# Kernel tuning notes

Measured on AMD Instinct MI355X. Metric: run time of the kernel, lower is better.

Reference implementation:

```python
import jax, jax.numpy as jnp
import numpy as np
from jax import lax

HID, FFN, NUM_EXPERTS, TOP_K = 1024, 4096, 16, 4
B, S = 4, 2048


def setup_inputs() -> dict:
    key = jax.random.key(0)
    ks = jax.random.split(key, 7)
    scale = 0.02
    x = jax.random.normal(ks[0], (B, S, HID), dtype=jnp.float32)
    Wg = jax.random.normal(ks[1], (HID, NUM_EXPERTS), dtype=jnp.float32) * scale
    bg = jnp.zeros((NUM_EXPERTS,), dtype=jnp.float32)
    W1 = jax.random.normal(ks[2], (NUM_EXPERTS, HID, FFN), dtype=jnp.float32) * scale
    b1 = jnp.zeros((NUM_EXPERTS, FFN), dtype=jnp.float32)
    W2 = jax.random.normal(ks[3], (NUM_EXPERTS, FFN, HID), dtype=jnp.float32) * scale
    b2 = jnp.zeros((NUM_EXPERTS, HID), dtype=jnp.float32)
    return {"x": x, "Wg": Wg, "bg": bg, "W1": W1, "b1": b1, "W2": W2, "b2": b2}


def reference(x, Wg, bg, W1, b1, W2, b2):
    b, s, h = x.shape
    xf = x.reshape(-1, h)                                  # [T, H]
    T = xf.shape[0]
    logits = xf @ Wg + bg                                  # [T, E]
    top_w, top_idx = lax.top_k(logits, TOP_K)              # [T, K]
    top_w = jax.nn.softmax(top_w, axis=-1)
    # Dense combine weights [T, E]; topk indices are distinct so add == set.
    combine = jnp.zeros((T, NUM_EXPERTS), dtype=xf.dtype)
    combine = combine.at[jnp.arange(T)[:, None], top_idx].add(top_w)

    def body(acc, params):
        W1e, b1e, W2e, b2e, ce = params                    # ce: [T]
        hdn = jax.nn.gelu(xf @ W1e + b1e, approximate=False)  # [T, F]
        ye = hdn @ W2e + b2e                               # [T, H]
        return acc + ce[:, None] * ye, None

    out, _ = lax.scan(body, jnp.zeros_like(xf), (W1, b1, W2, b2, combine.T))
    return out.reshape(b, s, h)
```

## Files before the change

### kernel.cpp

```cpp
#include <hip/hip_runtime.h>
#include <hip/hip_bf16.h>


#define HID 1024
#define FFN 4096
#define NE 16
#define TOPK 4
#define NTOK 8192
#define NPAIR (NTOK*TOPK)

typedef __attribute__((ext_vector_type(4))) float f32x4;
typedef __attribute__((ext_vector_type(8))) short bf16x8;
typedef unsigned short u16;
typedef unsigned int u32;

__device__ __forceinline__ u16 f2bf(float f){
  u32 u = __float_as_uint(f);
  u32 r = (u + 0x7fffu + ((u >> 16) & 1u)) >> 16;
  return (u16)r;
}

__device__ __forceinline__ void gload_lds16(const void* g, void* l){
  __builtin_amdgcn_global_load_lds((const __attribute__((address_space(1))) void*)g,
                                   (__attribute__((address_space(3))) void*)l, 16, 0, 0);
}

__global__ __launch_bounds__(256) void k_gating(const float* __restrict__ x,
    const float* __restrict__ Wg, const float* __restrict__ bg,
    int* __restrict__ counts, int* __restrict__ tke, float* __restrict__ tkw){
  int t    = (blockIdx.x << 2) + (threadIdx.x >> 6);
  int lane = threadIdx.x & 63;
  const float* xr = x + (size_t)t*HID + lane*16;
  float acc[NE];
  #pragma unroll
  for (int e=0;e<NE;e++) acc[e] = 0.f;
  #pragma unroll
  for (int j=0;j<16;j++){
    float xj = xr[j];
    const float* wr = Wg + (size_t)(lane*16 + j)*NE;
    #pragma unroll
    for (int e=0;e<NE;e++) acc[e] += xj * wr[e];
  }
  #pragma unroll
  for (int off=32; off; off>>=1){
    #pragma unroll
    for (int e=0;e<NE;e++) acc[e] += __shfl_xor(acc[e], off);
  }
  if (lane == 0){
    #pragma unroll
    for (int e=0;e<NE;e++) acc[e] += bg[e];
    int te[TOPK]; float tv[TOPK];
    #pragma unroll
    for (int k=0;k<TOPK;k++){
      int bi = 0; float bv = -1e30f;
      #pragma unroll
      for (int e=0;e<NE;e++) if (acc[e] > bv){ bv = acc[e]; bi = e; }
      te[k] = bi; tv[k] = bv; acc[bi] = -1e30f;
    }
    float m = tv[0], s = 0.f, w[TOPK];
    #pragma unroll
    for (int k=0;k<TOPK;k++){ w[k] = expf(tv[k]-m); s += w[k]; }
    float inv = 1.f/s;
    #pragma unroll
    for (int k=0;k<TOPK;k++){
      tke[t*TOPK+k] = te[k];
      tkw[t*TOPK+k] = w[k]*inv;
      atomicAdd(&counts[te[k]], 1);
    }
  }
}

__global__ void k_scan(const int* __restrict__ counts, int* __restrict__ offsets){
  if (threadIdx.x == 0){
    int a = 0;
    for (int e=0;e<NE;e++){ offsets[e] = a; a += counts[e]; }
    offsets[NE] = a;
  }
}

__global__ __launch_bounds__(256) void k_scatter(const int* __restrict__ tke,
    const float* __restrict__ tkw, const int* __restrict__ offsets,
    int* __restrict__ cursors, int* __restrict__ ltok, float* __restrict__ lw){
  int t = blockIdx.x*256 + threadIdx.x;
  #pragma unroll
  for (int k=0;k<TOPK;k++){
    int e = tke[t*TOPK+k];
    int p = atomicAdd(&cursors[e], 1);
    int r = offsets[e] + p;
    ltok[r] = t;
    lw[r]   = tkw[t*TOPK+k];
  }
}

__global__ __launch_bounds__(256) void k_cvt_x(const float* __restrict__ x, u16* __restrict__ xb){
  size_t i = ((size_t)blockIdx.x*256 + threadIdx.x) * 8;
  const float4* p = (const float4*)(x + i);
  float4 a = p[0], b = p[1];
  uint4 o;
  o.x = f2bf(a.x) | ((u32)f2bf(a.y) << 16);
  o.y = f2bf(a.z) | ((u32)f2bf(a.w) << 16);
  o.z = f2bf(b.x) | ((u32)f2bf(b.y) << 16);
  o.w = f2bf(b.z) | ((u32)f2bf(b.w) << 16);
  *(uint4*)(xb + i) = o;
}

__global__ __launch_bounds__(256) void k_wcvt(const float* __restrict__ src,
    u16* __restrict__ dst, int R, int C){
  int e = blockIdx.z;
  src += (size_t)e*R*C;
  dst += (size_t)e*R*C;
  int c0 = blockIdx.x*64, r0 = blockIdx.y*64;
  __shared__ u16 t[64][72];
  int tid = threadIdx.x;
  #pragma unroll
  for (int it=0; it<4; it++){
    int i  = it*256 + tid;
    int rr = i >> 4;
    int c4 = (i & 15) << 2;
    float4 v = *(const float4*)(src + (size_t)(r0+rr)*C + c0 + c4);
    t[rr][c4+0] = f2bf(v.x);
    t[rr][c4+1] = f2bf(v.y);
    t[rr][c4+2] = f2bf(v.z);
    t[rr][c4+3] = f2bf(v.w);
  }
  __syncthreads();
  #pragma unroll
  for (int it=0; it<2; it++){
    int i   = it*256 + tid;
    int cc  = i >> 3;
    int rr0 = (i & 7) << 3;
    uint4 o;
    o.x = (u32)t[rr0+0][cc] | ((u32)t[rr0+1][cc] << 16);
    o.y = (u32)t[rr0+2][cc] | ((u32)t[rr0+3][cc] << 16);
    o.z = (u32)t[rr0+4][cc] | ((u32)t[rr0+5][cc] << 16);
    o.w = (u32)t[rr0+6][cc] | ((u32)t[rr0+7][cc] << 16);
    *(uint4*)(dst + (size_t)(c0+cc)*R + r0 + rr0) = o;
  }
}

__global__ __launch_bounds__(256) void k_ffn1(
    const u16* __restrict__ xb, const u16* __restrict__ w1t,
    const float* __restrict__ b1,
    const int* __restrict__ counts, const int* __restrict__ offsets,
    const int* __restrict__ ltok, u16* __restrict__ hdn){
  int e = blockIdx.z;
  int cnt = counts[e];
  int row0 = blockIdx.y << 7;
  if (row0 >= cnt) return;
  int n0 = blockIdx.x << 7;
  int soff = offsets[e];
  const int* lt = ltok + soff;

  __shared__ u16 lA[128*64];
  __shared__ u16 lB[128*64];

  int tid = threadIdx.x, lane = tid & 63, wv = tid >> 6;
  int wr = (wv >> 1) << 6, wc = (wv & 1) << 6;
  int l15 = lane & 15, lkhi = (lane >> 4) << 3;

  f32x4 acc[4][4];
  #pragma unroll
  for (int m=0;m<4;m++){
    #pragma unroll
    for (int n=0;n<4;n++) acc[m][n] = (f32x4)0.f;
  }
  const u16* wBp = w1t + ((size_t)e*FFN + n0)*HID;

  for (int k0=0; k0<HID; k0+=64){
    __syncthreads();
    #pragma unroll
    for (int it=0; it<4; it++){
      int idx = it*256 + tid;
      int row = idx >> 3;
      int kc  = ((idx & 7) ^ (row & 7)) << 3;
      int rc = row0 + row; if (rc > cnt-1) rc = cnt-1;
      int tok = lt[rc];
      gload_lds16(xb  + (size_t)tok*HID + k0 + kc, &lA[idx<<3]);
      gload_lds16(wBp + (size_t)row*HID + k0 + kc, &lB[idx<<3]);
    }
    __syncthreads();
    #pragma unroll
    for (int kk=0; kk<64; kk+=32){
      bf16x8 af[4], bfv[4];
      #pragma unroll
      for (int m=0;m<4;m++){
        int ra = wr + m*16 + l15;
        af[m]  = *(const bf16x8*)&lA[ra*64 + ((kk + lkhi) ^ ((ra&7)<<3))];
      }
      #pragma unroll
      for (int n=0;n<4;n++){
        int rb = wc + n*16 + l15;
        bfv[n] = *(const bf16x8*)&lB[rb*64 + ((kk + lkhi) ^ ((rb&7)<<3))];
      }
      #pragma unroll
      for (int m=0;m<4;m++){
        #pragma unroll
        for (int n=0;n<4;n++)
          acc[m][n] = __builtin_amdgcn_mfma_f32_16x16x32_bf16(af[m], bfv[n], acc[m][n], 0,0,0);
      }
    }
  }
  int rhi = (lane >> 4) << 2;
  #pragma unroll
  for (int m=0;m<4;m++){
    int rl = wr + m*16 + rhi;
    #pragma unroll
    for (int j=0;j<4;j++){
      int row = row0 + rl + j;
      if (row < cnt){
        size_t base = (size_t)(soff + row)*FFN;
        #pragma unroll
        for (int n=0;n<4;n++){
          int col = n0 + wc + n*16 + l15;
          float z = acc[m][n][j] + b1[(size_t)e*FFN + col];
          float g = 0.5f*z*(1.0f + erff(z*0.70710678118654752f));
          hdn[base + col] = f2bf(g);
        }
      }
    }
  }
}

__global__ __launch_bounds__(256) void k_ffn2(
    const u16* __restrict__ hdn, const u16* __restrict__ w2t,
    const float* __restrict__ b2,
    const int* __restrict__ counts, const int* __restrict__ offsets,
    const int* __restrict__ ltok, const float* __restrict__ lw,
    float* __restrict__ out){
  int e = blockIdx.z;
  int cnt = counts[e];
  int row0 = blockIdx.y << 7;
  if (row0 >= cnt) return;
  int n0 = blockIdx.x << 7;
  int soff = offsets[e];

  __shared__ u16 lA[128*64];
  __shared__ u16 lB[128*64];

  int tid = threadIdx.x, lane = tid & 63, wv = tid >> 6;
  int wr = (wv >> 1) << 6, wc = (wv & 1) << 6;
  int l15 = lane & 15, lkhi = (lane >> 4) << 3;

  f32x4 acc[4][4];
  #pragma unroll
  for (int m=0;m<4;m++){
    #pragma unroll
    for (int n=0;n<4;n++) acc[m][n] = (f32x4)0.f;
  }
  const u16* wBp = w2t + ((size_t)e*HID + n0)*FFN;

  for (int k0=0; k0<FFN; k0+=64){
    __syncthreads();
    #pragma unroll
    for (int it=0; it<4; it++){
      int idx = it*256 + tid;
      int row = idx >> 3;
      int kc  = ((idx & 7) ^ (row & 7)) << 3;
      int rc = row0 + row; if (rc > cnt-1) rc = cnt-1;
      gload_lds16(hdn + (size_t)(soff+rc)*FFN + k0 + kc, &lA[idx<<3]);
      gload_lds16(wBp + (size_t)row*FFN     + k0 + kc, &lB[idx<<3]);
    }
    __syncthreads();
    #pragma unroll
    for (int kk=0; kk<64; kk+=32){
      bf16x8 af[4], bfv[4];
      #pragma unroll
      for (int m=0;m<4;m++){
        int ra = wr + m*16 + l15;
        af[m]  = *(const bf16x8*)&lA[ra*64 + ((kk + lkhi) ^ ((ra&7)<<3))];
      }
      #pragma unroll
      for (int n=0;n<4;n++){
        int rb = wc + n*16 + l15;
        bfv[n] = *(const bf16x8*)&lB[rb*64 + ((kk + lkhi) ^ ((rb&7)<<3))];
      }
      #pragma unroll
      for (int m=0;m<4;m++){
        #pragma unroll
        for (int n=0;n<4;n++)
          acc[m][n] = __builtin_amdgcn_mfma_f32_16x16x32_bf16(af[m], bfv[n], acc[m][n], 0,0,0);
      }
    }
  }
  int rhi = (lane >> 4) << 2;
  #pragma unroll
  for (int m=0;m<4;m++){
    int rl = wr + m*16 + rhi;
    #pragma unroll
    for (int j=0;j<4;j++){
      int row = row0 + rl + j;
      if (row < cnt){
        float sw = lw[soff+row];
        int tok  = ltok[soff+row];
        float* orow = out + (size_t)tok*HID;
        #pragma unroll
        for (int n=0;n<4;n++){
          int col = n0 + wc + n*16 + l15;
          atomicAdd(orow + col, sw*(acc[m][n][j] + b2[(size_t)e*HID + col]));
        }
      }
    }
  }
}

extern "C" void kernel_launch(void* const* d_in, const int* in_sizes, int n_in,
                              void* d_out, int out_size, void* d_ws, size_t ws_size,
                              hipStream_t stream){
  const float* x  = (const float*)d_in[0];
  const float* Wg = (const float*)d_in[1];
  const float* bg = (const float*)d_in[2];
  const float* W1 = (const float*)d_in[3];
  const float* b1 = (const float*)d_in[4];
  const float* W2 = (const float*)d_in[5];
  const float* b2 = (const float*)d_in[6];
  float* out = (float*)d_out;

  char* ws = (char*)d_ws;
  size_t off = 0;
  u16* SLOT_A = (u16*)(ws + off); off += (size_t)NE*FFN*HID*2;
  u16* XB  = (u16*)(ws + off); off += (size_t)NTOK*HID*2;
  u16* HDN = (u16*)(ws + off); off += (size_t)NPAIR*FFN*2;
  int*   LTOK = (int*)(ws + off);   off += (size_t)NPAIR*4;
  float* LW   = (float*)(ws + off); off += (size_t)NPAIR*4;
  int*   TKE  = (int*)(ws + off);   off += (size_t)NPAIR*4;
  float* TKW  = (float*)(ws + off); off += (size_t)NPAIR*4;
  int*   CTRL = (int*)(ws + off);   off += 256;
  int* counts  = CTRL;
  int* offsets = CTRL + 16;
  int* cursors = CTRL + 33;

  (void)hipMemsetAsync(CTRL, 0, 256, stream);
  (void)hipMemsetAsync(out, 0, (size_t)NTOK*HID*sizeof(float), stream);

  k_gating<<<NTOK/4, 256, 0, stream>>>(x, Wg, bg, counts, TKE, TKW);
  k_scan<<<1, 64, 0, stream>>>(counts, offsets);
  k_scatter<<<NTOK/256, 256, 0, stream>>>(TKE, TKW, offsets, cursors, LTOK, LW);
  k_cvt_x<<<(NTOK*HID/8)/256, 256, 0, stream>>>(x, XB);
  k_wcvt<<<dim3(FFN/64, HID/64, NE), 256, 0, stream>>>(W1, SLOT_A, HID, FFN);
  k_ffn1<<<dim3(FFN/128, NTOK/128, NE), 256, 0, stream>>>(XB, SLOT_A, b1, counts, offsets, LTOK, HDN);
  k_wcvt<<<dim3(HID/64, FFN/64, NE), 256, 0, stream>>>(W2, SLOT_A, FFN, HID);
  k_ffn2<<<dim3(HID/128, NTOK/128, NE), 256, 0, stream>>>(HDN, SLOT_A, b2, counts, offsets, LTOK, LW, out);
}
```

Baseline: 2.298 ms.

## Double-buffer LDS tiles in both expert FFN GEMM kernels to overlap loads

Both grouped GEMM kernels now use two LDS buffers per operand. Each iteration issues the global-to-LDS loads for the next K tile before running the MFMAs on the current one, and synchronises once per iteration instead of twice. Per-thread gather offsets, including the token index lookup, are precomputed once outside the K loop. LDS use doubles to 64 KB per block, which may cut the number of resident blocks. Correctness depends on the compiler's waitcnt handling of async LDS loads at the barrier.

Result: no change. 2.323 ms (+1.1%).

```diff
diff --git a/kernel.cpp b/kernel.cpp
--- a/kernel.cpp
+++ b/kernel.cpp
@@ -151,8 +151,8 @@
   int soff = offsets[e];
   const int* lt = ltok + soff;
 
-  __shared__ u16 lA[128*64];
-  __shared__ u16 lB[128*64];
+  __shared__ u16 lA[2][128*64];
+  __shared__ u16 lB[2][128*64];
 
   int tid = threadIdx.x, lane = tid & 63, wv = tid >> 6;
   int wr = (wv >> 1) << 6, wc = (wv & 1) << 6;
@@ -166,31 +166,43 @@
   }
   const u16* wBp = w1t + ((size_t)e*FFN + n0)*HID;
 
-  for (int k0=0; k0<HID; k0+=64){
-    __syncthreads();
+  size_t aoff[4], boff[4];
+  #pragma unroll
+  for (int it=0; it<4; it++){
+    int idx = it*256 + tid;
+    int row = idx >> 3;
+    int kc  = ((idx & 7) ^ (row & 7)) << 3;
+    int rc = row0 + row; if (rc > cnt-1) rc = cnt-1;
+    aoff[it] = (size_t)lt[rc]*HID + kc;
+    boff[it] = (size_t)row*HID + kc;
+  }
+
+  auto stage = [&](int buf, int k0v){
     #pragma unroll
     for (int it=0; it<4; it++){
       int idx = it*256 + tid;
-      int row = idx >> 3;
-      int kc  = ((idx & 7) ^ (row & 7)) << 3;
-      int rc = row0 + row; if (rc > cnt-1) rc = cnt-1;
-      int tok = lt[rc];
-      gload_lds16(xb  + (size_t)tok*HID + k0 + kc, &lA[idx<<3]);
-      gload_lds16(wBp + (size_t)row*HID + k0 + kc, &lB[idx<<3]);
-    }
-    __syncthreads();
+      gload_lds16(xb  + aoff[it] + k0v, &lA[buf][idx<<3]);
+      gload_lds16(wBp + boff[it] + k0v, &lB[buf][idx<<3]);
+    }
+  };
+
+  stage(0, 0);
+  __syncthreads();
+  int cur = 0;
+  for (int t=0; t<HID/64; ++t){
+    if (t+1 < HID/64) stage(cur^1, (t+1)*64);
     #pragma unroll
     for (int kk=0; kk<64; kk+=32){
       bf16x8 af[4], bfv[4];
       #pragma unroll
       for (int m=0;m<4;m++){
         int ra = wr + m*16 + l15;
-        af[m]  = *(const bf16x8*)&lA[ra*64 + ((kk + lkhi) ^ ((ra&7)<<3))];
+        af[m]  = *(const bf16x8*)&lA[cur][ra*64 + ((kk + lkhi) ^ ((ra&7)<<3))];
       }
       #pragma unroll
       for (int n=0;n<4;n++){
         int rb = wc + n*16 + l15;
-        bfv[n] = *(const bf16x8*)&lB[rb*64 + ((kk + lkhi) ^ ((rb&7)<<3))];
+        bfv[n] = *(const bf16x8*)&lB[cur][rb*64 + ((kk + lkhi) ^ ((rb&7)<<3))];
       }
       #pragma unroll
       for (int m=0;m<4;m++){
@@ -199,6 +211,8 @@
           acc[m][n] = __builtin_amdgcn_mfma_f32_16x16x32_bf16(af[m], bfv[n], acc[m][n], 0,0,0);
       }
     }
+    __syncthreads();
+    cur ^= 1;
   }
   int rhi = (lane >> 4) << 2;
   #pragma unroll
@@ -234,8 +248,8 @@
   int n0 = blockIdx.x << 7;
   int soff = offsets[e];
 
-  __shared__ u16 lA[128*64];
-  __shared__ u16 lB[128*64];
+  __shared__ u16 lA[2][128*64];
+  __shared__ u16 lB[2][128*64];
 
   int tid = threadIdx.x, lane = tid & 63, wv = tid >> 6;
   int wr = (wv >> 1) << 6, wc = (wv & 1) << 6;
@@ -249,30 +263,43 @@
   }
   const u16* wBp = w2t + ((size_t)e*HID + n0)*FFN;
 
-  for (int k0=0; k0<FFN; k0+=64){
-    __syncthreads();
+  size_t aoff[4], boff[4];
+  #pragma unroll
+  for (int it=0; it<4; it++){
+    int idx = it*256 + tid;
+    int row = idx >> 3;
+    int kc  = ((idx & 7) ^ (row & 7)) << 3;
+    int rc = row0 + row; if (rc > cnt-1) rc = cnt-1;
+    aoff[it] = (size_t)(soff+rc)*FFN + kc;
+    boff[it] = (size_t)row*FFN + kc;
+  }
+
+  auto stage = [&](int buf, int k0v){
     #pragma unroll
     for (int it=0; it<4; it++){
       int idx = it*256 + tid;
-      int row = idx >> 3;
-      int kc  = ((idx & 7) ^ (row & 7)) << 3;
-      int rc = row0 + row; if (rc > cnt-1) rc = cnt-1;
-      gload_lds16(hdn + (size_t)(soff+rc)*FFN + k0 + kc, &lA[idx<<3]);
-      gload_lds16(wBp + (size_t)row*FFN     + k0 + kc, &lB[idx<<3]);
-    }
-    __syncthreads();
+      gload_lds16(hdn + aoff[it] + k0v, &lA[buf][idx<<3]);
+      gload_lds16(wBp + boff[it] + k0v, &lB[buf][idx<<3]);
+    }
+  };
+
+  stage(0, 0);
+  __syncthreads();
+  int cur = 0;
+  for (int t=0; t<FFN/64; ++t){
+    if (t+1 < FFN/64) stage(cur^1, (t+1)*64);
     #pragma unroll
     for (int kk=0; kk<64; kk+=32){
       bf16x8 af[4], bfv[4];
       #pragma unroll
       for (int m=0;m<4;m++){
         int ra = wr + m*16 + l15;
-        af[m]  = *(const bf16x8*)&lA[ra*64 + ((kk + lkhi) ^ ((ra&7)<<3))];
+        af[m]  = *(const bf16x8*)&lA[cur][ra*64 + ((kk + lkhi) ^ ((ra&7)<<3))];
       }
       #pragma unroll
       for (int n=0;n<4;n++){
         int rb = wc + n*16 + l15;
-        bfv[n] = *(const bf16x8*)&lB[rb*64 + ((kk + lkhi) ^ ((rb&7)<<3))];
+        bfv[n] = *(const bf16x8*)&lB[cur][rb*64 + ((kk + lkhi) ^ ((rb&7)<<3))];
       }
       #pragma unroll
       for (int m=0;m<4;m++){
@@ -281,6 +308,8 @@
           acc[m][n] = __builtin_amdgcn_mfma_f32_16x16x32_bf16(af[m], bfv[n], acc[m][n], 0,0,0);
       }
     }
+    __syncthreads();
+    cur ^= 1;
   }
   int rhi = (lane >> 4) << 2;
   #pragma unroll
```
